# Kernel optimization log

Hardware: AMD Instinct MI355X
Metric: run time of the kernel (lower is better)

Reference implementation:

```python
import jax, jax.numpy as jnp
import numpy as np

G, N, K, F = 256, 512, 6, 64  # graphs, nodes/graph, knn k, n_features
T = G * N

def leaky(x):
    return jnp.where(x >= 0, x, 0.2 * x)

def prelu(x, a):
    return jnp.where(x >= 0, x, a * x)

def knn_idx(x):
    # per-graph kNN (k=6, self excluded); idx[i] = global indices of 6 nearest nbrs of i
    xg = x.reshape(G, N, F)
    sq = jnp.sum(xg * xg, axis=-1)                       # [G,N]
    d = sq[:, :, None] + sq[:, None, :] - 2.0 * jnp.einsum('gnf,gmf->gnm', xg, xg)
    d = jnp.where(jnp.eye(N, dtype=bool)[None], jnp.inf, d)  # loop=False
    _, idx = jax.lax.top_k(-d, K)                        # [G,N,K] local indices
    idx = idx + (jnp.arange(G) * N)[:, None, None]       # make global
    return idx.reshape(T, K)

def gconv(h, idx, W, b):
    # PyG GeneralConv defaults: out[i] = sum_{j in nbr(i)} (x_j W + b) + x_i
    s = jnp.take(h, idx, axis=0).sum(axis=1)             # [T,F] sum of neighbor feats
    return s @ W + K * b + h

def forward(x, W1, b1, a1, W2, b2, a2,
            Wc1, bc1, Wc2, bc2, Wc3, bc3, Wc4, bc4,
            W3, b3, a3, W4, b4, a4,
            Wh1, bh1, Wh2, bh2, Wh3, bh3, Wh4, bh4, idx):
    h = prelu(x @ W1 + b1, a1)
    h = prelu(h @ W2 + b2, a2)
    h = gconv(h, idx, Wc1, bc1)
    h = gconv(h, idx, Wc2, bc2)
    h = gconv(h, idx, Wc3, bc3)
    h = gconv(h, idx, Wc4, bc4)
    h = prelu(h @ W3 + b3, a3)
    h = prelu(h @ W4 + b4, a4)
    pooled = h.reshape(G, N, F).sum(axis=1)              # global_add_pool -> [G,F]
    y = leaky(pooled @ Wh1 + bh1)
    y = leaky(y @ Wh2 + bh2)
    y = leaky(y @ Wh3 + bh3)
    return y @ Wh4 + bh4                                 # [G,1]

def setup_inputs():
    key = jax.random.key(0)
    ks = jax.random.split(key, 16)
    def lin(k, i, o):
        k1, k2 = jax.random.split(k)
        s = 1.0 / np.sqrt(i)
        return (jax.random.uniform(k1, (i, o), jnp.float32, -s, s),
                jax.random.uniform(k2, (o,), jnp.float32, -s, s))
    inp = {"x": jax.random.normal(ks[0], (T, F), jnp.float32)}
    W1, b1 = lin(ks[1], F, F); W2, b2 = lin(ks[2], F, F)
    Wc1, bc1 = lin(ks[3], F, F); Wc2, bc2 = lin(ks[4], F, F)
    Wc3, bc3 = lin(ks[5], F, F); Wc4, bc4 = lin(ks[6], F, F)
    W3, b3 = lin(ks[7], F, F); W4, b4 = lin(ks[8], F, F)
    Wh1, bh1 = lin(ks[9], F, 4 * F); Wh2, bh2 = lin(ks[10], 4 * F, 4 * F)
    Wh3, bh3 = lin(ks[11], 4 * F, F); Wh4, bh4 = lin(ks[12], F, 1)
    a = 0.25 * jnp.ones((F,), jnp.float32)  # PReLU init
    inp.update(W1=W1, b1=b1, a1=a, W2=W2, b2=b2, a2=a,
               Wc1=Wc1, bc1=bc1, Wc2=Wc2, bc2=bc2, Wc3=Wc3, bc3=bc3, Wc4=Wc4, bc4=bc4,
               W3=W3, b3=b3, a3=a, W4=W4, b4=b4, a4=a,
               Wh1=Wh1, bh1=bh1, Wh2=Wh2, bh2=bh2, Wh3=Wh3, bh3=bh3, Wh4=Wh4, bh4=bh4)
    return inp

def reference(x, W1, b1, a1, W2, b2, a2, Wc1, bc1, Wc2, bc2, Wc3, bc3, Wc4, bc4,
              W3, b3, a3, W4, b4, a4, Wh1, bh1, Wh2, bh2, Wh3, bh3, Wh4, bh4):
    idx = knn_idx(x)  # edge_index built from raw x, as in the torch module
    return forward(x, W1, b1, a1, W2, b2, a2, Wc1, bc1, Wc2, bc2, Wc3, bc3, Wc4, bc4,
                   W3, b3, a3, W4, b4, a4, Wh1, bh1, Wh2, bh2, Wh3, bh3, Wh4, bh4, idx)
```

## Files before the change

kernel.cpp:

```cpp
#include <hip/hip_runtime.h>

#define NGRAPH 256
#define NNODE  512
#define KNN    6
#define NCAND  12
#define NF     64
#define SBF    72
#define NT     768
#define NW     12
#define PBF    18432
#define CANDO  PBF
#define SQO    (PBF + 3072)
#define WTO    36864
#define NBRO   39168
#define LDS_FLOATS 40704
#define LDS_BYTES  (LDS_FLOATS*4)
#define POOLP  PBF
#define POOLED (PBF + 1024)
#define Y1OFF  (PBF + 1088)
#define Y2OFF  (PBF + 1344)
#define BIG 1e30f

typedef float v4f __attribute__((ext_vector_type(4)));
typedef float v2f __attribute__((ext_vector_type(2)));
typedef short v8s __attribute__((ext_vector_type(8)));

struct Params {
  const float *x;
  const float *W1,*b1,*a1, *W2,*b2,*a2;
  const float *Wc0,*bc0, *Wc1,*bc1, *Wc2,*bc2, *Wc3,*bc3;
  const float *W3,*b3,*a3, *W4,*b4,*a4;
  const float *Wh1,*bh1, *Wh2,*bh2, *Wh3,*bh3, *Wh4,*bh4;
  float *out;
};

__device__ __forceinline__ unsigned f2bf(float x) {
  union { float f; unsigned u; } cc; cc.f = x;
  unsigned u = cc.u;
  return (u + 0x7FFFu + ((u >> 16) & 1u)) >> 16;
}
__device__ __forceinline__ float bflo(unsigned u) {
  union { unsigned u; float f; } c; c.u = u << 16; return c.f;
}
__device__ __forceinline__ float bfhi(unsigned u) {
  union { unsigned u; float f; } c; c.u = u & 0xffff0000u; return c.f;
}
__device__ __forceinline__ v2f up2(unsigned u) {
  v2f r; r.x = bflo(u); r.y = bfhi(u); return r;
}

__device__ __forceinline__ v8s bfrag(const unsigned short* base, int row, int c0) {
  return *(const v8s*)(base + row*SBF + c0);
}

__device__ __forceinline__ float packe(float e, int j) {
  return __uint_as_float((__float_as_uint(e) & 0xFFFFFE00u) | (unsigned)j);
}

__device__ __forceinline__ void ins8(float (&b)[8], float v) {
  if (v < b[7]) {
#pragma unroll
    for (int p = 0; p < 8; ++p) {
      float lo = fminf(b[p], v);
      v = fmaxf(b[p], v);
      b[p] = lo;
    }
  }
}
__device__ __forceinline__ void ins12(float (&b)[NCAND], float v) {
  if (v < b[NCAND-1]) {
#pragma unroll
    for (int p = 0; p < NCAND; ++p) {
      float lo = fminf(b[p], v);
      v = fmaxf(b[p], v);
      b[p] = lo;
    }
  }
}

__device__ __forceinline__ void stage_wt(const float* W, unsigned short* wt, int tid) {
  const int col = tid >> 3, ks = (tid & 7) * 8;
  const float* wp = W + col;
  unsigned d[4];
#pragma unroll
  for (int i = 0; i < 4; ++i) {
    unsigned lo = f2bf(wp[(ks + 2*i    ) * NF]);
    unsigned hi = f2bf(wp[(ks + 2*i + 1) * NF]);
    d[i] = lo | (hi << 16);
  }
  *(uint4*)&wt[col*SBF + ks] = make_uint4(d[0], d[1], d[2], d[3]);
}

template<int NTILE>
__device__ __forceinline__ void filter_tiles(const unsigned short* hbf,
                                             const float* ldsf,
                                             unsigned short* cand,
                                             const int (&tts)[NTILE],
                                             int lane, int c, int qq) {
  v8s A0[NTILE], A1[NTILE];
  float d8[NTILE][8];
  int i0[NTILE];
#pragma unroll
  for (int k = 0; k < NTILE; ++k) {
    i0[k] = tts[k] * 16;
    A0[k] = bfrag(hbf, i0[k] + c, qq*8);
    A1[k] = bfrag(hbf, i0[k] + c, 32 + qq*8);
#pragma unroll
    for (int m = 0; m < 8; ++m) d8[k][m] = BIG;
  }
#pragma unroll 1
  for (int jt = 0; jt < 32; ++jt) {
    const int j0 = jt * 16;
    v8s B0 = bfrag(hbf, j0 + c, qq*8);
    v8s B1 = bfrag(hbf, j0 + c, 32 + qq*8);
    float4 sv = *(const float4*)&ldsf[SQO + j0 + qq*4];
    const int jb = j0 + qq*4;
#pragma unroll
    for (int k = 0; k < NTILE; ++k) {
      v4f acc = {0.f, 0.f, 0.f, 0.f};
      acc = __builtin_amdgcn_mfma_f32_16x16x32_bf16(B0, A0[k], acc, 0, 0, 0);
      acc = __builtin_amdgcn_mfma_f32_16x16x32_bf16(B1, A1[k], acc, 0, 0, 0);
      float e0 = fmaf(-2.f, acc[0], sv.x);
      float e1 = fmaf(-2.f, acc[1], sv.y);
      float e2 = fmaf(-2.f, acc[2], sv.z);
      float e3 = fmaf(-2.f, acc[3], sv.w);
      if (jt == tts[k]) {
        const int myrow = i0[k] + c;
        if (jb     == myrow) e0 = BIG;
        if (jb + 1 == myrow) e1 = BIG;
        if (jb + 2 == myrow) e2 = BIG;
        if (jb + 3 == myrow) e3 = BIG;
      }
      ins8(d8[k], packe(e0, jb));
      ins8(d8[k], packe(e1, jb+1));
      ins8(d8[k], packe(e2, jb+2));
      ins8(d8[k], packe(e3, jb+3));
    }
  }
#pragma unroll
  for (int k = 0; k < NTILE; ++k) {
    float cd[NCAND];
#pragma unroll
    for (int m = 0; m < 8; ++m) cd[m] = d8[k][m];
#pragma unroll
    for (int m = 8; m < NCAND; ++m) cd[m] = BIG;
    {
      float pd[8];
#pragma unroll
      for (int s = 0; s < 8; ++s) pd[s] = __shfl_xor(cd[s], 16);
#pragma unroll
      for (int s = 0; s < 8; ++s) ins12(cd, pd[s]);
    }
    {
      float pd[NCAND];
#pragma unroll
      for (int s = 0; s < NCAND; ++s) pd[s] = __shfl_xor(cd[s], 32);
#pragma unroll
      for (int s = 0; s < NCAND; ++s) ins12(cd, pd[s]);
    }
    if (lane < 16) {
#pragma unroll
      for (int s = 0; s < NCAND; ++s)
        cand[(i0[k] + lane)*NCAND + s] =
          (unsigned short)(__float_as_uint(cd[s]) & 0x1FFu);
    }
  }
}

__global__ __launch_bounds__(NT) void fused_gnn(Params P) {
  extern __shared__ float lds[];
  unsigned short* hbf  = (unsigned short*)lds;
  unsigned short* pbf  = (unsigned short*)&lds[PBF];
  unsigned short* wt   = (unsigned short*)&lds[WTO];
  unsigned short* cand = (unsigned short*)&lds[CANDO];
  unsigned short* nbrs = (unsigned short*)&lds[NBRO];
  const int tid  = threadIdx.x;
  const int g    = blockIdx.x;
  const int rA   = tid;
  const int lane = tid & 63;
  const int w    = tid >> 6;
  const int c    = lane & 15;
  const int qq   = lane >> 4;

  const float* xgp = P.x + (size_t)g * NNODE * NF;
  const float4* xg = (const float4*)xgp;

#pragma unroll 1
  for (int i = tid; i < NNODE*NF/4; i += NT) {
    float4 v = xg[i];
    int row = i >> 4, k4 = i & 15;
    unsigned lo = f2bf(v.x) | (f2bf(v.y) << 16);
    unsigned hi = f2bf(v.z) | (f2bf(v.w) << 16);
    *(uint2*)&hbf[row*SBF + 4*k4] = make_uint2(lo, hi);
  }
  __syncthreads();

  if (tid < 512) {
    const uint4* xr = (const uint4*)(hbf + rA*SBF);
    float s = 0.f;
#pragma unroll
    for (int k = 0; k < 8; ++k) {
      uint4 u = xr[k];
      float f;
      f = bflo(u.x); s = fmaf(f, f, s); f = bfhi(u.x); s = fmaf(f, f, s);
      f = bflo(u.y); s = fmaf(f, f, s); f = bfhi(u.y); s = fmaf(f, f, s);
      f = bflo(u.z); s = fmaf(f, f, s); f = bfhi(u.z); s = fmaf(f, f, s);
      f = bflo(u.w); s = fmaf(f, f, s); f = bfhi(u.w); s = fmaf(f, f, s);
    }
    lds[SQO + rA] = s;
  }
  __syncthreads();

  if (w < 8) {
    int tts[3] = {w, w + 8, w + 16};
    filter_tiles<3>(hbf, lds, cand, tts, lane, c, qq);
  } else {
    int tts[2] = {w + 16, w + 20};
    filter_tiles<2>(hbf, lds, cand, tts, lane, c, qq);
  }
  __syncthreads();

  if (tid < 512) {
    const float4* xrow = (const float4*)(xgp + rA*NF);
    float s0 = 0.f;
#pragma unroll
    for (int k4 = 0; k4 < 16; ++k4) {
      float4 a = xrow[k4];
      s0 = fmaf(a.x,a.x,s0); s0 = fmaf(a.y,a.y,s0); s0 = fmaf(a.z,a.z,s0); s0 = fmaf(a.w,a.w,s0);
    }
    lds[SQO + rA] = s0;
  }
  __syncthreads();

  if (tid < 512) {
    const float4* xrow = (const float4*)(xgp + rA*NF);
    float nd[6]; int ni[6];
#pragma unroll
    for (int m = 0; m < 6; ++m) { nd[m] = BIG; ni[m] = 0x7fffffff; }
    int cnd[NCAND];
#pragma unroll
    for (int s = 0; s < NCAND; ++s) cnd[s] = cand[rA*NCAND + s];

#pragma unroll 1
    for (int s = 0; s < NCAND; ++s) {
      int j = cnd[s];
      const float4* xj = (const float4*)(xgp + j*NF);
      float4 aa = {0.f, 0.f, 0.f, 0.f};
#pragma unroll
      for (int k4 = 0; k4 < 16; ++k4) {
        float4 a = xrow[k4];
        float4 v = xj[k4];
        aa.x = fmaf(a.x, v.x, aa.x); aa.y = fmaf(a.y, v.y, aa.y);
        aa.z = fmaf(a.z, v.z, aa.z); aa.w = fmaf(a.w, v.w, aa.w);
      }
      float e = fmaf(-2.f, (aa.x+aa.y)+(aa.z+aa.w), lds[SQO + j]);
      if (e < nd[5] || (e == nd[5] && j < ni[5])) {
#pragma unroll
        for (int pp = 0; pp < 6; ++pp) {
          bool lt = (e < nd[pp]) || (e == nd[pp] && j < ni[pp]);
          float tb2 = nd[pp]; int ti = ni[pp];
          nd[pp] = lt ? e : tb2;  ni[pp] = lt ? j : ti;
          e      = lt ? tb2 : e;  j      = lt ? ti : j;
        }
      }
    }
#pragma unroll
    for (int m = 0; m < 6; ++m) nbrs[rA*KNN + m] = (unsigned short)ni[m];
  }

#pragma unroll 1
  for (int L = 0; L < 8; ++L) {
    const bool isconv = (L >= 2 && L <= 5);
    const float* Wl = L==0?P.W1 : L==1?P.W2 : L==2?P.Wc0 : L==3?P.Wc1 :
                      L==4?P.Wc2 : L==5?P.Wc3 : L==6?P.W3 : P.W4;
    const float* bl = L==0?P.b1 : L==1?P.b2 : L==2?P.bc0 : L==3?P.bc1 :
                      L==4?P.bc2 : L==5?P.bc3 : L==6?P.b3 : P.b4;
    const float* al = L==0?P.a1 : L==1?P.a2 : L==6?P.a3 : P.a4;

    __syncthreads();
    if (tid < 512) stage_wt(Wl, wt, tid);
    __syncthreads();

    v8s B0[4], B1[4];
#pragma unroll
    for (int n = 0; n < 4; ++n) {
      B0[n] = bfrag(wt, n*16 + c, qq*8);
      B1[n] = bfrag(wt, n*16 + c, 32 + qq*8);
    }
    float br[4], ar[4];
    if (!isconv) {
#pragma unroll
      for (int n = 0; n < 4; ++n) { br[n] = bl[n*16 + c]; ar[n] = al[n*16 + c]; }
    }

#pragma unroll 1
    for (int tt = w; tt < 32; tt += NW) {
      const int i0 = tt * 16;
      v8s A0 = bfrag(hbf, i0 + c, qq*8);
      v8s A1 = bfrag(hbf, i0 + c, 32 + qq*8);
#pragma unroll
      for (int n = 0; n < 4; ++n) {
        v4f acc = {0.f, 0.f, 0.f, 0.f};
        acc = __builtin_amdgcn_mfma_f32_16x16x32_bf16(A0, B0[n], acc, 0, 0, 0);
        acc = __builtin_amdgcn_mfma_f32_16x16x32_bf16(A1, B1[n], acc, 0, 0, 0);
        if (isconv) {
#pragma unroll
          for (int r = 0; r < 4; ++r)
            pbf[(i0 + qq*4 + r)*SBF + n*16 + c] = (unsigned short)f2bf(acc[r]);
        } else {
#pragma unroll
          for (int r = 0; r < 4; ++r) {
            float v = acc[r] + br[n];
            v = v >= 0.f ? v : ar[n]*v;
            hbf[(i0 + qq*4 + r)*SBF + n*16 + c] = (unsigned short)f2bf(v);
          }
        }
      }
    }

    if (isconv) {
      __syncthreads();
      {
        const int s = tid & 7;
        const float* bls = bl + 8*s;
        float4 bv0 = *(const float4*)(bls);
        float4 bv1 = *(const float4*)(bls + 4);
#pragma unroll 1
        for (int r = tid >> 3; r < NNODE; r += NT/8) {
          const unsigned short* nb = &nbrs[r*KNN];
          uint4 own = *(const uint4*)&hbf[r*SBF + 8*s];
          v2f a0 = up2(own.x), a1 = up2(own.y), a2 = up2(own.z), a3 = up2(own.w);
          v2f t;
          t.x = bv0.x; t.y = bv0.y; a0 += 6.f*t;
          t.x = bv0.z; t.y = bv0.w; a1 += 6.f*t;
          t.x = bv1.x; t.y = bv1.y; a2 += 6.f*t;
          t.x = bv1.z; t.y = bv1.w; a3 += 6.f*t;
#pragma unroll
          for (int mm = 0; mm < KNN; ++mm) {
            int nbr = nb[mm];
            uint4 p = *(const uint4*)&pbf[nbr*SBF + 8*s];
            a0 += up2(p.x); a1 += up2(p.y); a2 += up2(p.z); a3 += up2(p.w);
          }
          uint4 o;
          o.x = f2bf(a0.x) | (f2bf(a0.y) << 16);
          o.y = f2bf(a1.x) | (f2bf(a1.y) << 16);
          o.z = f2bf(a2.x) | (f2bf(a2.y) << 16);
          o.w = f2bf(a3.x) | (f2bf(a3.y) << 16);
          *(uint4*)&hbf[r*SBF + 8*s] = o;
        }
      }
    }
  }
  __syncthreads();

  if (tid < 512) {
    int f2 = tid & 31, cch = tid >> 5;
    int rstart = cch * 32;
    const unsigned* h32 = (const unsigned*)hbf;
    v2f s2; s2.x = 0.f; s2.y = 0.f;
#pragma unroll 1
    for (int r = 0; r < 32; ++r) s2 += up2(h32[(rstart + r)*(SBF/2) + f2]);
    *(float2*)&lds[POOLP + cch*64 + 2*f2] = make_float2(s2.x, s2.y);
  }
  __syncthreads();
  if (tid < 64) {
    float pool = 0.f;
#pragma unroll
    for (int cc = 0; cc < 16; ++cc) pool += lds[POOLP + cc*64 + tid];
    lds[POOLED + tid] = pool;
  }
  __syncthreads();

  if (tid < 256) {
    float acc = P.bh1[tid];
#pragma unroll 4
    for (int k = 0; k < 64; ++k) acc = fmaf(lds[POOLED+k], P.Wh1[k*256 + tid], acc);
    lds[Y1OFF + tid] = acc >= 0.f ? acc : 0.2f*acc;
  }
  __syncthreads();
  if (tid < 512) {
    int o = tid & 255, hh = tid >> 8;
    float acc = hh ? 0.f : P.bh2[o];
    const int k0 = hh * 128;
#pragma unroll 4
    for (int k = k0; k < k0 + 128; ++k) acc = fmaf(lds[Y1OFF+k], P.Wh2[k*256 + o], acc);
    lds[POOLP + hh*256 + o] = acc;
  }
  __syncthreads();
  if (tid < 256) {
    float acc = lds[POOLP + tid] + lds[POOLP + 256 + tid];
    lds[Y2OFF + tid] = acc >= 0.f ? acc : 0.2f*acc;
  }
  __syncthreads();
  if (tid < 256) {
    int o = tid & 63, hh = tid >> 6;
    float acc = 0.f;
    const int k0 = hh * 64;
#pragma unroll 4
    for (int k = k0; k < k0 + 64; ++k) acc = fmaf(lds[Y2OFF+k], P.Wh3[k*64 + o], acc);
    lds[POOLP + hh*64 + o] = acc;
  }
  __syncthreads();
  if (tid < 64) {
    float acc = P.bh3[tid] + lds[POOLP + tid] + lds[POOLP + 64 + tid]
              + lds[POOLP + 128 + tid] + lds[POOLP + 192 + tid];
    float y3 = acc >= 0.f ? acc : 0.2f*acc;
    float v = y3 * P.Wh4[tid];
#pragma unroll
    for (int off = 32; off >= 1; off >>= 1) v += __shfl_down(v, off);
    if (tid == 0) P.out[g] = v + P.bh4[0];
  }
}

extern "C" void kernel_launch(void* const* d_in, const int* in_sizes, int n_in,
                              void* d_out, int out_size, void* d_ws, size_t ws_size,
                              hipStream_t stream) {
  Params P;
  P.x   = (const float*)d_in[0];
  P.W1  = (const float*)d_in[1];  P.b1  = (const float*)d_in[2];  P.a1 = (const float*)d_in[3];
  P.W2  = (const float*)d_in[4];  P.b2  = (const float*)d_in[5];  P.a2 = (const float*)d_in[6];
  P.Wc0 = (const float*)d_in[7];  P.bc0 = (const float*)d_in[8];
  P.Wc1 = (const float*)d_in[9];  P.bc1 = (const float*)d_in[10];
  P.Wc2 = (const float*)d_in[11]; P.bc2 = (const float*)d_in[12];
  P.Wc3 = (const float*)d_in[13]; P.bc3 = (const float*)d_in[14];
  P.W3  = (const float*)d_in[15]; P.b3  = (const float*)d_in[16]; P.a3 = (const float*)d_in[17];
  P.W4  = (const float*)d_in[18]; P.b4  = (const float*)d_in[19]; P.a4 = (const float*)d_in[20];
  P.Wh1 = (const float*)d_in[21]; P.bh1 = (const float*)d_in[22];
  P.Wh2 = (const float*)d_in[23]; P.bh2 = (const float*)d_in[24];
  P.Wh3 = (const float*)d_in[25]; P.bh3 = (const float*)d_in[26];
  P.Wh4 = (const float*)d_in[27]; P.bh4 = (const float*)d_in[28];
  P.out = (float*)d_out;

  (void)hipFuncSetAttribute(reinterpret_cast<const void*>(fused_gnn),
                            hipFuncAttributeMaxDynamicSharedMemorySize, LDS_BYTES);

  fused_gnn<<<NGRAPH, NT, LDS_BYTES, stream>>>(P);
}
```

Measured before the change: 308.7 us.

## Prefetch next layer weights into registers and cache query row for kNN refine

Weight staging is software-pipelined: the next layer's weights are loaded into registers before the current layer's MFMA work, then written to shared memory after the B fragments are read, with sync points reorganised so one barrier pair per layer is replaced. The query row for the exact kNN refinement is kept in 16 float4 registers instead of being reloaded from global memory for every candidate. Together these aim to hide global-load latency for weights and to cut redundant row loads, at the cost of extra register pressure (64 floats plus 8 for prefetch) and a riskier ordering of barriers around the shared weight buffer.

```diff
diff --git a/kernel.cpp b/kernel.cpp
--- a/kernel.cpp
+++ b/kernel.cpp
@@ -78,16 +78,18 @@
   }
 }
 
-__device__ __forceinline__ void stage_wt(const float* W, unsigned short* wt, int tid) {
+__device__ __forceinline__ void ld8(const float* W, float (&wf)[8], int tid) {
   const int col = tid >> 3, ks = (tid & 7) * 8;
   const float* wp = W + col;
+#pragma unroll
+  for (int i = 0; i < 8; ++i) wf[i] = wp[(ks + i) * NF];
+}
+__device__ __forceinline__ void wt_write(const float (&wf)[8], unsigned short* wt, int tid) {
+  const int col = tid >> 3, ks = (tid & 7) * 8;
   unsigned d[4];
 #pragma unroll
-  for (int i = 0; i < 4; ++i) {
-    unsigned lo = f2bf(wp[(ks + 2*i    ) * NF]);
-    unsigned hi = f2bf(wp[(ks + 2*i + 1) * NF]);
-    d[i] = lo | (hi << 16);
-  }
+  for (int i = 0; i < 4; ++i)
+    d[i] = f2bf(wf[2*i]) | (f2bf(wf[2*i+1]) << 16);
   *(uint4*)&wt[col*SBF + ks] = make_uint4(d[0], d[1], d[2], d[3]);
 }
 
@@ -220,12 +222,15 @@
   }
   __syncthreads();
 
+  float4 xr16[16];
   if (tid < 512) {
     const float4* xrow = (const float4*)(xgp + rA*NF);
+#pragma unroll
+    for (int k4 = 0; k4 < 16; ++k4) xr16[k4] = xrow[k4];
     float s0 = 0.f;
 #pragma unroll
     for (int k4 = 0; k4 < 16; ++k4) {
-      float4 a = xrow[k4];
+      float4 a = xr16[k4];
       s0 = fmaf(a.x,a.x,s0); s0 = fmaf(a.y,a.y,s0); s0 = fmaf(a.z,a.z,s0); s0 = fmaf(a.w,a.w,s0);
     }
     lds[SQO + rA] = s0;
@@ -233,7 +238,6 @@
   __syncthreads();
 
   if (tid < 512) {
-    const float4* xrow = (const float4*)(xgp + rA*NF);
     float nd[6]; int ni[6];
 #pragma unroll
     for (int m = 0; m < 6; ++m) { nd[m] = BIG; ni[m] = 0x7fffffff; }
@@ -248,10 +252,9 @@
       float4 aa = {0.f, 0.f, 0.f, 0.f};
 #pragma unroll
       for (int k4 = 0; k4 < 16; ++k4) {
-        float4 a = xrow[k4];
         float4 v = xj[k4];
-        aa.x = fmaf(a.x, v.x, aa.x); aa.y = fmaf(a.y, v.y, aa.y);
-        aa.z = fmaf(a.z, v.z, aa.z); aa.w = fmaf(a.w, v.w, aa.w);
+        aa.x = fmaf(xr16[k4].x, v.x, aa.x); aa.y = fmaf(xr16[k4].y, v.y, aa.y);
+        aa.z = fmaf(xr16[k4].z, v.z, aa.z); aa.w = fmaf(xr16[k4].w, v.w, aa.w);
       }
       float e = fmaf(-2.f, (aa.x+aa.y)+(aa.z+aa.w), lds[SQO + j]);
       if (e < nd[5] || (e == nd[5] && j < ni[5])) {
@@ -268,19 +271,19 @@
     for (int m = 0; m < 6; ++m) nbrs[rA*KNN + m] = (unsigned short)ni[m];
   }
 
+  float wf[8];
+  if (tid < 512) ld8(P.W1, wf, tid);
+  __syncthreads();
+  if (tid < 512) { wt_write(wf, wt, tid); ld8(P.W2, wf, tid); }
+  __syncthreads();
+
 #pragma unroll 1
   for (int L = 0; L < 8; ++L) {
     const bool isconv = (L >= 2 && L <= 5);
-    const float* Wl = L==0?P.W1 : L==1?P.W2 : L==2?P.Wc0 : L==3?P.Wc1 :
-                      L==4?P.Wc2 : L==5?P.Wc3 : L==6?P.W3 : P.W4;
     const float* bl = L==0?P.b1 : L==1?P.b2 : L==2?P.bc0 : L==3?P.bc1 :
                       L==4?P.bc2 : L==5?P.bc3 : L==6?P.b3 : P.b4;
     const float* al = L==0?P.a1 : L==1?P.a2 : L==6?P.a3 : P.a4;
 
-    __syncthreads();
-    if (tid < 512) stage_wt(Wl, wt, tid);
-    __syncthreads();
-
     v8s B0[4], B1[4];
 #pragma unroll
     for (int n = 0; n < 4; ++n) {
@@ -291,6 +294,16 @@
     if (!isconv) {
 #pragma unroll
       for (int n = 0; n < 4; ++n) { br[n] = bl[n*16 + c]; ar[n] = al[n*16 + c]; }
+    }
+    __syncthreads();
+
+    if (tid < 512 && L < 7) {
+      wt_write(wf, wt, tid);
+      if (L < 6) {
+        const float* Wn2 = L==0?P.Wc0 : L==1?P.Wc1 : L==2?P.Wc2 :
+                           L==3?P.Wc3 : L==4?P.W3 : P.W4;
+        ld8(Wn2, wf, tid);
+      }
     }
 
 #pragma unroll 1
@@ -317,37 +330,35 @@
         }
       }
     }
+    __syncthreads();
 
     if (isconv) {
-      __syncthreads();
-      {
-        const int s = tid & 7;
-        const float* bls = bl + 8*s;
-        float4 bv0 = *(const float4*)(bls);
-        float4 bv1 = *(const float4*)(bls + 4);
-#pragma unroll 1
-        for (int r = tid >> 3; r < NNODE; r += NT/8) {
-          const unsigned short* nb = &nbrs[r*KNN];
-          uint4 own = *(const uint4*)&hbf[r*SBF + 8*s];
-          v2f a0 = up2(own.x), a1 = up2(own.y), a2 = up2(own.z), a3 = up2(own.w);
-          v2f t;
-          t.x = bv0.x; t.y = bv0.y; a0 += 6.f*t;
-          t.x = bv0.z; t.y = bv0.w; a1 += 6.f*t;
-          t.x = bv1.x; t.y = bv1.y; a2 += 6.f*t;
-          t.x = bv1.z; t.y = bv1.w; a3 += 6.f*t;
-#pragma unroll
-          for (int mm = 0; mm < KNN; ++mm) {
-            int nbr = nb[mm];
-            uint4 p = *(const uint4*)&pbf[nbr*SBF + 8*s];
-            a0 += up2(p.x); a1 += up2(p.y); a2 += up2(p.z); a3 += up2(p.w);
-          }
-          uint4 o;
-          o.x = f2bf(a0.x) | (f2bf(a0.y) << 16);
-          o.y = f2bf(a1.x) | (f2bf(a1.y) << 16);
-          o.z = f2bf(a2.x) | (f2bf(a2.y) << 16);
-          o.w = f2bf(a3.x) | (f2bf(a3.y) << 16);
-          *(uint4*)&hbf[r*SBF + 8*s] = o;
+      const int s = tid & 7;
+      const float* bls = bl + 8*s;
+      float4 bv0 = *(const float4*)(bls);
+      float4 bv1 = *(const float4*)(bls + 4);
+#pragma unroll 1
+      for (int r = tid >> 3; r < NNODE; r += NT/8) {
+        const unsigned short* nb = &nbrs[r*KNN];
+        uint4 own = *(const uint4*)&hbf[r*SBF + 8*s];
+        v2f a0 = up2(own.x), a1 = up2(own.y), a2 = up2(own.z), a3 = up2(own.w);
+        v2f t;
+        t.x = bv0.x; t.y = bv0.y; a0 += 6.f*t;
+        t.x = bv0.z; t.y = bv0.w; a1 += 6.f*t;
+        t.x = bv1.x; t.y = bv1.y; a2 += 6.f*t;
+        t.x = bv1.z; t.y = bv1.w; a3 += 6.f*t;
+#pragma unroll
+        for (int mm = 0; mm < KNN; ++mm) {
+          int nbr = nb[mm];
+          uint4 p = *(const uint4*)&pbf[nbr*SBF + 8*s];
+          a0 += up2(p.x); a1 += up2(p.y); a2 += up2(p.z); a3 += up2(p.w);
         }
+        uint4 o;
+        o.x = f2bf(a0.x) | (f2bf(a0.y) << 16);
+        o.y = f2bf(a1.x) | (f2bf(a1.y) << 16);
+        o.z = f2bf(a2.x) | (f2bf(a2.y) << 16);
+        o.w = f2bf(a3.x) | (f2bf(a3.y) << 16);
+        *(uint4*)&hbf[r*SBF + 8*s] = o;
       }
     }
   }
```

Measured after the change: 301.4 us. -2.4%, faster.
